# Kernel tuning notes

Measured on AMD Instinct MI355X. Metric: run time of the kernel, lower is better.

Reference implementation:

```python
import jax, jax.numpy as jnp
import numpy as np

N_DATA = 200000   # num_data
DIM = 128         # input_dim
BATCH = 40000     # minibatch receptive-field nodes (rows of output, cols of subsampled_support)
E_SUB = 320000    # nnz of subsampled_support (avg sampled degree 8)
E_SUP = 1280000   # nnz of support rows for the batch (avg degree 32)


def setup_inputs() -> dict:
    key = jax.random.key(0)
    ks = jax.random.split(key, 9)
    inputs = jax.random.normal(ks[0], (BATCH, DIM), dtype=jnp.float32)
    # old cached activations (non-trainable variable, but a float tensor)
    old_activation = jax.random.normal(ks[1], (N_DATA, DIM), dtype=jnp.float32)
    input_fields = jax.random.randint(ks[2], (BATCH,), 0, N_DATA, dtype=jnp.int32)
    # subsampled_support: sparse [BATCH, BATCH] in COO
    sub_rows = jax.random.randint(ks[3], (E_SUB,), 0, BATCH, dtype=jnp.int32)
    sub_cols = jax.random.randint(ks[4], (E_SUB,), 0, BATCH, dtype=jnp.int32)
    sub_vals = jax.random.uniform(ks[5], (E_SUB,), dtype=jnp.float32)
    # support: sparse [BATCH, N_DATA] in COO
    sup_rows = jax.random.randint(ks[6], (E_SUP,), 0, BATCH, dtype=jnp.int32)
    sup_cols = jax.random.randint(ks[7], (E_SUP,), 0, N_DATA, dtype=jnp.int32)
    sup_vals = jax.random.uniform(ks[8], (E_SUP,), dtype=jnp.float32)
    return {
        "inputs": inputs,
        "old_activation": old_activation,
        "input_fields": input_fields,
        "sub_rows": sub_rows,
        "sub_cols": sub_cols,
        "sub_vals": sub_vals,
        "sup_rows": sup_rows,
        "sup_cols": sup_cols,
        "sup_vals": sup_vals,
    }


def _spmm(rows, cols, vals, dense, num_rows):
    # sparse [num_rows, K] (COO) @ dense [K, D] -> [num_rows, D]
    return jax.ops.segment_sum(vals[:, None] * dense[cols], rows, num_segments=num_rows)


def reference(inputs, old_activation, input_fields, sub_rows, sub_cols, sub_vals,
              sup_rows, sup_cols, sup_vals):
    M = inputs.shape[0]
    old = old_activation[input_fields]                      # [B, D] gather
    norm = lambda x: jnp.sqrt(jnp.sum(jnp.square(x)))
    sim = jnp.sum(inputs * old) / norm(inputs) / norm(old)  # logged scalar (tf.Print)
    diff = inputs - old
    out = _spmm(sub_rows, sub_cols, sub_vals, diff, M) \
        + _spmm(sup_rows, sup_cols, sup_vals, old_activation, M)
    return out, sim
```

## Files before the change

kernel.cpp:

```cpp
#include <hip/hip_runtime.h>
#include <math.h>

#define DIM 128
#define TPB 256
#define PREP_GRID 2048
#define SUB_CAP 32
#define SUP_CAP 64
#define OVER_MAX 65536

__global__ void prep_bin_kernel(const float* __restrict__ inputs,
                                const float* __restrict__ old_act,
                                const int* __restrict__ fields,
                                const int* __restrict__ sub_rows, const int* __restrict__ sub_cols,
                                const float* __restrict__ sub_vals, int e_sub,
                                const int* __restrict__ sup_rows, const int* __restrict__ sup_cols,
                                const float* __restrict__ sup_vals, int e_sup,
                                int* __restrict__ cnt,
                                int2* __restrict__ pk_sub, int2* __restrict__ pk_sup,
                                int4* __restrict__ over,
                                float* __restrict__ partials, float* __restrict__ diff,
                                int use_diff, int nrows, int n2) {
    int tid = blockIdx.x * blockDim.x + threadIdx.x;
    int stride = gridDim.x * blockDim.x;
    int* over_cnt = cnt + 2 * nrows;

    float dot = 0.f, nx = 0.f, ny = 0.f;
    for (int i = tid; i < n2; i += stride) {
        int idx = i * 2;
        int b = idx >> 7, d = idx & (DIM - 1);
        float2 x = *(const float2*)(inputs + idx);
        int f = fields[b];
        float2 y = *(const float2*)(old_act + (size_t)f * DIM + d);
        dot += x.x * y.x + x.y * y.y;
        nx  += x.x * x.x + x.y * x.y;
        ny  += y.x * y.x + y.y * y.y;
        if (use_diff)
            *(float2*)(diff + idx) = make_float2(x.x - y.x, x.y - y.y);
    }
    int e_tot = e_sub + e_sup;
    for (int i = tid; i < e_tot; i += stride) {
        int r, c, sup; float v;
        if (i < e_sub) { r = sub_rows[i]; c = sub_cols[i]; v = sub_vals[i]; sup = 0; }
        else { int k = i - e_sub; r = sup_rows[k]; c = sup_cols[k]; v = sup_vals[k]; sup = 1; }
        int pos = atomicAdd(&cnt[sup ? nrows + r : r], 1);
        int cap = sup ? SUP_CAP : SUB_CAP;
        if (pos < cap) {
            int2* base = sup ? (pk_sup + (size_t)r * SUP_CAP) : (pk_sub + (size_t)r * SUB_CAP);
            base[pos] = make_int2(c, __float_as_int(v));
        } else {
            int op = atomicAdd(over_cnt, 1);
            if (op < OVER_MAX) over[op] = make_int4(r, c, __float_as_int(v), sup);
        }
    }
    for (int off = 32; off > 0; off >>= 1) {
        dot += __shfl_down(dot, off, 64);
        nx  += __shfl_down(nx,  off, 64);
        ny  += __shfl_down(ny,  off, 64);
    }
    __shared__ float s[3][4];
    int lane = threadIdx.x & 63, wv = threadIdx.x >> 6;
    if (lane == 0) { s[0][wv] = dot; s[1][wv] = nx; s[2][wv] = ny; }
    __syncthreads();
    if (threadIdx.x == 0) {
        float D = 0.f, NX = 0.f, NY = 0.f;
        for (int w = 0; w < 4; ++w) { D += s[0][w]; NX += s[1][w]; NY += s[2][w]; }
        partials[blockIdx.x * 3 + 0] = D;
        partials[blockIdx.x * 3 + 1] = NX;
        partials[blockIdx.x * 3 + 2] = NY;
    }
}

__global__ void row_bucket_kernel(const int* __restrict__ cnt,
                                  const int2* __restrict__ pk_sub, const int2* __restrict__ pk_sup,
                                  const float* __restrict__ diff,
                                  const float* __restrict__ inputs, const float* __restrict__ old_act,
                                  const int* __restrict__ fields,
                                  float* __restrict__ out, int nrows, int use_diff) {
    int wv = threadIdx.x >> 6, lane = threadIdx.x & 63;
    int r = blockIdx.x * (blockDim.x >> 6) + wv;
    if (r >= nrows) return;
    const int d0 = lane * 2;
    float a0 = 0.f, a1 = 0.f;

    {
        int e = cnt[r]; if (e > SUB_CAP) e = SUB_CAP;
        const int2* bp = pk_sub + (size_t)r * SUB_CAP;
        if (use_diff) {
            int j = 0;
            for (; j + 4 <= e; j += 4) {
                int2 p0 = bp[j], p1 = bp[j + 1], p2 = bp[j + 2], p3 = bp[j + 3];
                float2 y0 = *(const float2*)(diff + (size_t)p0.x * DIM + d0);
                float2 y1 = *(const float2*)(diff + (size_t)p1.x * DIM + d0);
                float2 y2 = *(const float2*)(diff + (size_t)p2.x * DIM + d0);
                float2 y3 = *(const float2*)(diff + (size_t)p3.x * DIM + d0);
                a0 += __int_as_float(p0.y) * y0.x; a1 += __int_as_float(p0.y) * y0.y;
                a0 += __int_as_float(p1.y) * y1.x; a1 += __int_as_float(p1.y) * y1.y;
                a0 += __int_as_float(p2.y) * y2.x; a1 += __int_as_float(p2.y) * y2.y;
                a0 += __int_as_float(p3.y) * y3.x; a1 += __int_as_float(p3.y) * y3.y;
            }
            for (; j < e; ++j) {
                int2 p = bp[j];
                float2 y = *(const float2*)(diff + (size_t)p.x * DIM + d0);
                a0 += __int_as_float(p.y) * y.x;
                a1 += __int_as_float(p.y) * y.y;
            }
        } else {
            for (int j = 0; j < e; ++j) {
                int2 p = bp[j];
                int c = p.x; float v = __int_as_float(p.y);
                int f = fields[c];
                float2 x = *(const float2*)(inputs  + (size_t)c * DIM + d0);
                float2 y = *(const float2*)(old_act + (size_t)f * DIM + d0);
                a0 += v * (x.x - y.x);
                a1 += v * (x.y - y.y);
            }
        }
    }
    {
        int e = cnt[nrows + r]; if (e > SUP_CAP) e = SUP_CAP;
        const int2* bp = pk_sup + (size_t)r * SUP_CAP;
        int j = 0;
        for (; j + 4 <= e; j += 4) {
            int2 p0 = bp[j], p1 = bp[j + 1], p2 = bp[j + 2], p3 = bp[j + 3];
            float2 y0 = *(const float2*)(old_act + (size_t)p0.x * DIM + d0);
            float2 y1 = *(const float2*)(old_act + (size_t)p1.x * DIM + d0);
            float2 y2 = *(const float2*)(old_act + (size_t)p2.x * DIM + d0);
            float2 y3 = *(const float2*)(old_act + (size_t)p3.x * DIM + d0);
            a0 += __int_as_float(p0.y) * y0.x; a1 += __int_as_float(p0.y) * y0.y;
            a0 += __int_as_float(p1.y) * y1.x; a1 += __int_as_float(p1.y) * y1.y;
            a0 += __int_as_float(p2.y) * y2.x; a1 += __int_as_float(p2.y) * y2.y;
            a0 += __int_as_float(p3.y) * y3.x; a1 += __int_as_float(p3.y) * y3.y;
        }
        for (; j < e; ++j) {
            int2 p = bp[j];
            float2 y = *(const float2*)(old_act + (size_t)p.x * DIM + d0);
            a0 += __int_as_float(p.y) * y.x;
            a1 += __int_as_float(p.y) * y.y;
        }
    }
    *(float2*)(out + (size_t)r * DIM + d0) = make_float2(a0, a1);
}

__global__ void tail_kernel(const float* __restrict__ partials, int np,
                            const int* __restrict__ cnt, const int4* __restrict__ over,
                            const float* __restrict__ diff,
                            const float* __restrict__ inputs, const float* __restrict__ old_act,
                            const int* __restrict__ fields,
                            float* __restrict__ out, int nrows, int n, int use_diff) {
    if (blockIdx.x == 0 && threadIdx.x < 64) {
        double dot = 0.0, nx = 0.0, ny = 0.0;
        for (int i = threadIdx.x; i < np; i += 64) {
            dot += (double)partials[i * 3 + 0];
            nx  += (double)partials[i * 3 + 1];
            ny  += (double)partials[i * 3 + 2];
        }
        for (int off = 32; off > 0; off >>= 1) {
            dot += __shfl_down(dot, off, 64);
            nx  += __shfl_down(nx,  off, 64);
            ny  += __shfl_down(ny,  off, 64);
        }
        if (threadIdx.x == 0)
            out[n] = (float)(dot / (sqrt(nx) * sqrt(ny)));
    }
    int no = cnt[2 * nrows]; if (no > OVER_MAX) no = OVER_MAX;
    int tid = blockIdx.x * blockDim.x + threadIdx.x;
    int stride = gridDim.x * blockDim.x;
    for (int i = tid; i < no; i += stride) {
        int4 t = over[i];
        int r = t.x, c = t.y, sup = t.w;
        float v = __int_as_float(t.z);
        for (int d = 0; d < DIM; ++d) {
            float term;
            if (sup) term = old_act[(size_t)c * DIM + d];
            else if (use_diff) term = diff[(size_t)c * DIM + d];
            else term = inputs[(size_t)c * DIM + d] - old_act[(size_t)fields[c] * DIM + d];
            atomicAdd(&out[(size_t)r * DIM + d], v * term);
        }
    }
}

__global__ void prep4_kernel(const float* __restrict__ inputs, const float* __restrict__ old_act,
                             const int* __restrict__ fields,
                             const int* __restrict__ sub_rows, int e_sub,
                             const int* __restrict__ sup_rows, int e_sup,
                             int* __restrict__ cnt, float* __restrict__ partials,
                             int nrows, int n2) {
    int tid = blockIdx.x * blockDim.x + threadIdx.x;
    int stride = gridDim.x * blockDim.x;
    float dot = 0.f, nx = 0.f, ny = 0.f;
    for (int i = tid; i < n2; i += stride) {
        int idx = i * 2;
        int b = idx >> 7, d = idx & (DIM - 1);
        float2 x = *(const float2*)(inputs + idx);
        int f = fields[b];
        float2 y = *(const float2*)(old_act + (size_t)f * DIM + d);
        dot += x.x * y.x + x.y * y.y;
        nx  += x.x * x.x + x.y * x.y;
        ny  += y.x * y.x + y.y * y.y;
    }
    int e_tot = e_sub + e_sup;
    for (int i = tid; i < e_tot; i += stride) {
        int r = (i < e_sub) ? sub_rows[i] : (nrows + sup_rows[i - e_sub]);
        atomicAdd(&cnt[r], 1);
    }
    for (int off = 32; off > 0; off >>= 1) {
        dot += __shfl_down(dot, off, 64);
        nx  += __shfl_down(nx,  off, 64);
        ny  += __shfl_down(ny,  off, 64);
    }
    __shared__ float s[3][4];
    int lane = threadIdx.x & 63, wv = threadIdx.x >> 6;
    if (lane == 0) { s[0][wv] = dot; s[1][wv] = nx; s[2][wv] = ny; }
    __syncthreads();
    if (threadIdx.x == 0) {
        float D = 0.f, NX = 0.f, NY = 0.f;
        for (int w = 0; w < 4; ++w) { D += s[0][w]; NX += s[1][w]; NY += s[2][w]; }
        partials[blockIdx.x * 3 + 0] = D;
        partials[blockIdx.x * 3 + 1] = NX;
        partials[blockIdx.x * 3 + 2] = NY;
    }
}

__global__ void finalize4_kernel(const float* __restrict__ partials, int np,
                                 float* __restrict__ out_sim) {
    double dot = 0.0, nx = 0.0, ny = 0.0;
    for (int i = threadIdx.x; i < np; i += 64) {
        dot += (double)partials[i * 3 + 0];
        nx  += (double)partials[i * 3 + 1];
        ny  += (double)partials[i * 3 + 2];
    }
    for (int off = 32; off > 0; off >>= 1) {
        dot += __shfl_down(dot, off, 64);
        nx  += __shfl_down(nx,  off, 64);
        ny  += __shfl_down(ny,  off, 64);
    }
    if (threadIdx.x == 0)
        *out_sim = (float)(dot / (sqrt(nx) * sqrt(ny)));
}

__global__ void scanA_kernel(const int* __restrict__ cnt, int* __restrict__ tmp,
                             int* __restrict__ bsum, int m) {
    __shared__ int s[256];
    int i = blockIdx.x * 256 + threadIdx.x;
    int v = (i < m) ? cnt[i] : 0;
    s[threadIdx.x] = v;
    __syncthreads();
    for (int d = 1; d < 256; d <<= 1) {
        int t = (threadIdx.x >= (unsigned)d) ? s[threadIdx.x - d] : 0;
        __syncthreads();
        s[threadIdx.x] += t;
        __syncthreads();
    }
    if (i < m) tmp[i] = s[threadIdx.x] - v;
    if (threadIdx.x == 255) bsum[blockIdx.x] = s[255];
}

__global__ void scanB_kernel(int* __restrict__ bsum, int* __restrict__ boff, int nb) {
    __shared__ int s[512];
    int v = (threadIdx.x < nb) ? bsum[threadIdx.x] : 0;
    s[threadIdx.x] = v;
    __syncthreads();
    for (int d = 1; d < 512; d <<= 1) {
        int t = (threadIdx.x >= (unsigned)d) ? s[threadIdx.x - d] : 0;
        __syncthreads();
        s[threadIdx.x] += t;
        __syncthreads();
    }
    if (threadIdx.x < nb) boff[threadIdx.x] = s[threadIdx.x] - v;
}

__global__ void scanC_kernel(const int* tmp, const int* __restrict__ boff,
                             int* __restrict__ off, int* cur, int m, int e_tot) {
    int i = blockIdx.x * 256 + threadIdx.x;
    if (i < m) {
        int o = tmp[i] + boff[i >> 8];
        off[i] = o;
        cur[i] = o;
    }
    if (i == 0) off[m] = e_tot;
}

__global__ void scatter4_kernel(const int* __restrict__ sub_rows, const int* __restrict__ sub_cols,
                                const float* __restrict__ sub_vals, int e_sub,
                                const int* __restrict__ sup_rows, const int* __restrict__ sup_cols,
                                const float* __restrict__ sup_vals, int e_sup,
                                int* __restrict__ cur, int2* __restrict__ pk, int nrows) {
    int i = blockIdx.x * blockDim.x + threadIdx.x;
    int e_tot = e_sub + e_sup;
    if (i >= e_tot) return;
    int r, c; float v;
    if (i < e_sub) { r = sub_rows[i]; c = sub_cols[i]; v = sub_vals[i]; }
    else { int k = i - e_sub; r = nrows + sup_rows[k]; c = sup_cols[k]; v = sup_vals[k]; }
    int pos = atomicAdd(&cur[r], 1);
    pk[pos] = make_int2(c, __float_as_int(v));
}

__global__ void row4_kernel(const int* __restrict__ off, const int2* __restrict__ pk,
                            const float* __restrict__ inputs, const float* __restrict__ old_act,
                            const int* __restrict__ fields, float* __restrict__ out, int nrows) {
    int wv = threadIdx.x >> 6, lane = threadIdx.x & 63;
    int r = blockIdx.x * (blockDim.x >> 6) + wv;
    if (r >= nrows) return;
    int d0 = lane * 2;
    float a0 = 0.f, a1 = 0.f;
    int b = off[r], e = off[r + 1];
    for (int j = b; j < e; ++j) {
        int2 p = pk[j];
        int c = p.x; float v = __int_as_float(p.y);
        int f = fields[c];
        float2 x = *(const float2*)(inputs  + (size_t)c * DIM + d0);
        float2 y = *(const float2*)(old_act + (size_t)f * DIM + d0);
        a0 += v * (x.x - y.x);
        a1 += v * (x.y - y.y);
    }
    b = off[nrows + r]; e = off[nrows + r + 1];
    for (int j = b; j < e; ++j) {
        int2 p = pk[j];
        int c = p.x; float v = __int_as_float(p.y);
        float2 y = *(const float2*)(old_act + (size_t)c * DIM + d0);
        a0 += v * y.x;
        a1 += v * y.y;
    }
    *(float2*)(out + (size_t)r * DIM + d0) = make_float2(a0, a1);
}

extern "C" void kernel_launch(void* const* d_in, const int* in_sizes, int n_in,
                              void* d_out, int out_size, void* d_ws, size_t ws_size,
                              hipStream_t stream) {
    const float* inputs   = (const float*)d_in[0];
    const float* old_act  = (const float*)d_in[1];
    const int*   fields   = (const int*)d_in[2];
    const int*   sub_rows = (const int*)d_in[3];
    const int*   sub_cols = (const int*)d_in[4];
    const float* sub_vals = (const float*)d_in[5];
    const int*   sup_rows = (const int*)d_in[6];
    const int*   sup_cols = (const int*)d_in[7];
    const float* sup_vals = (const float*)d_in[8];

    const int n     = in_sizes[0];
    const int nrows = n / DIM;
    const int e_sub = in_sizes[3];
    const int e_sup = in_sizes[6];
    const int e_tot = e_sub + e_sup;

    float* out = (float*)d_out;
    char*  ws  = (char*)d_ws;

    size_t off_part = 0;
    size_t off_cnt  = (PREP_GRID * 3 * 4 + 63) & ~(size_t)63;
    size_t off_over = (off_cnt + (size_t)(2 * nrows + 1) * 4 + 15) & ~(size_t)15;
    size_t off_psub = off_over + (size_t)OVER_MAX * 16;
    size_t off_psup = off_psub + (size_t)nrows * SUB_CAP * 8;
    size_t off_diff = off_psup + (size_t)nrows * SUP_CAP * 8;
    size_t need_base = off_diff;
    size_t need_diff = off_diff + (size_t)n * 4;

    if (ws_size >= need_base) {
        float* partials = (float*)(ws + off_part);
        int*   cnt      = (int*)(ws + off_cnt);
        int4*  over     = (int4*)(ws + off_over);
        int2*  pk_sub   = (int2*)(ws + off_psub);
        int2*  pk_sup   = (int2*)(ws + off_psup);
        float* diff     = (float*)(ws + off_diff);
        int use_diff    = (ws_size >= need_diff) ? 1 : 0;

        hipMemsetAsync(cnt, 0, (size_t)(2 * nrows + 1) * 4, stream);

        prep_bin_kernel<<<PREP_GRID, TPB, 0, stream>>>(
            inputs, old_act, fields,
            sub_rows, sub_cols, sub_vals, e_sub,
            sup_rows, sup_cols, sup_vals, e_sup,
            cnt, pk_sub, pk_sup, over, partials, diff, use_diff, nrows, n / 2);

        row_bucket_kernel<<<(nrows + 3) / 4, TPB, 0, stream>>>(
            cnt, pk_sub, pk_sup, diff, inputs, old_act, fields, out, nrows, use_diff);

        tail_kernel<<<32, TPB, 0, stream>>>(
            partials, PREP_GRID, cnt, over, diff, inputs, old_act, fields,
            out, nrows, n, use_diff);
        return;
    }

    const int m     = 2 * nrows;
    const int nblkA = (m + 255) / 256;
    size_t f_part = 0;
    size_t f_cnt  = (2048 * 3 * 4 + 63) & ~(size_t)63;
    size_t f_tmp  = f_cnt + (size_t)m * 4;
    size_t f_offs = f_tmp + (size_t)m * 4;
    size_t f_bsum = f_offs + (size_t)(m + 1) * 4;
    size_t f_boff = f_bsum + 4096;
    size_t f_pk   = (f_boff + 4096 + 7) & ~(size_t)7;
    size_t f_need = f_pk + (size_t)e_tot * 8;

    float* partials = (float*)(ws + f_part);
    int*   cnt      = (int*)(ws + f_cnt);
    int*   tmp      = (int*)(ws + f_tmp);
    int*   offs     = (int*)(ws + f_offs);
    int*   bsum     = (int*)(ws + f_bsum);
    int*   boff     = (int*)(ws + f_boff);
    int2*  pk       = (int2*)(ws + f_pk);

    if (ws_size >= f_need && nblkA <= 512) {
        hipMemsetAsync(cnt, 0, (size_t)m * 4, stream);
        prep4_kernel<<<2048, 256, 0, stream>>>(inputs, old_act, fields,
                                               sub_rows, e_sub, sup_rows, e_sup,
                                               cnt, partials, nrows, n / 2);
        scanA_kernel<<<nblkA, 256, 0, stream>>>(cnt, tmp, bsum, m);
        scanB_kernel<<<1, 512, 0, stream>>>(bsum, boff, nblkA);
        scanC_kernel<<<nblkA, 256, 0, stream>>>(tmp, boff, offs, tmp, m, e_tot);
        scatter4_kernel<<<(e_tot + 255) / 256, 256, 0, stream>>>(
            sub_rows, sub_cols, sub_vals, e_sub,
            sup_rows, sup_cols, sup_vals, e_sup, tmp, pk, nrows);
        row4_kernel<<<(nrows + 3) / 4, 256, 0, stream>>>(offs, pk, inputs, old_act,
                                                         fields, out, nrows);
        finalize4_kernel<<<1, 64, 0, stream>>>(partials, 2048, out + n);
    }
}
```

Measured before the change: 419.8 us.

## Partition COO binning by row across XCD groups and widen loads

The binning loop now splits blocks into 8 groups keyed on blockIdx low bits. Each group scans all edge rows but only inserts edges whose row matches its group, so atomics and bucket writes for a row stay on one XCD's L2. The cost is that every group rereads the row arrays, which is 8x traffic on the row indices. The prep gather now moves float4 instead of float2, and the row bucket kernel reads packed (col,val) pairs as int4 with the sup loop unrolled to 8 in-flight gathers.

```diff
diff --git a/kernel.cpp b/kernel.cpp
--- a/kernel.cpp
+++ b/kernel.cpp
@@ -7,6 +7,7 @@
 #define SUB_CAP 32
 #define SUP_CAP 64
 #define OVER_MAX 65536
+#define NXCD 8
 
 __global__ void prep_bin_kernel(const float* __restrict__ inputs,
                                 const float* __restrict__ old_act,
@@ -19,29 +20,38 @@
                                 int2* __restrict__ pk_sub, int2* __restrict__ pk_sup,
                                 int4* __restrict__ over,
                                 float* __restrict__ partials, float* __restrict__ diff,
-                                int use_diff, int nrows, int n2) {
+                                int use_diff, int nrows, int n4) {
     int tid = blockIdx.x * blockDim.x + threadIdx.x;
     int stride = gridDim.x * blockDim.x;
     int* over_cnt = cnt + 2 * nrows;
 
     float dot = 0.f, nx = 0.f, ny = 0.f;
-    for (int i = tid; i < n2; i += stride) {
-        int idx = i * 2;
+    for (int i = tid; i < n4; i += stride) {
+        int idx = i * 4;
         int b = idx >> 7, d = idx & (DIM - 1);
-        float2 x = *(const float2*)(inputs + idx);
+        float4 x = *(const float4*)(inputs + idx);
         int f = fields[b];
-        float2 y = *(const float2*)(old_act + (size_t)f * DIM + d);
-        dot += x.x * y.x + x.y * y.y;
-        nx  += x.x * x.x + x.y * x.y;
-        ny  += y.x * y.x + y.y * y.y;
+        float4 y = *(const float4*)(old_act + (size_t)f * DIM + d);
+        dot += x.x * y.x + x.y * y.y + x.z * y.z + x.w * y.w;
+        nx  += x.x * x.x + x.y * x.y + x.z * x.z + x.w * x.w;
+        ny  += y.x * y.x + y.y * y.y + y.z * y.z + y.w * y.w;
         if (use_diff)
-            *(float2*)(diff + idx) = make_float2(x.x - y.x, x.y - y.y);
-    }
+            *(float4*)(diff + idx) = make_float4(x.x - y.x, x.y - y.y, x.z - y.z, x.w - y.w);
+    }
+
     int e_tot = e_sub + e_sup;
-    for (int i = tid; i < e_tot; i += stride) {
-        int r, c, sup; float v;
-        if (i < e_sub) { r = sub_rows[i]; c = sub_cols[i]; v = sub_vals[i]; sup = 0; }
-        else { int k = i - e_sub; r = sup_rows[k]; c = sup_cols[k]; v = sup_vals[k]; sup = 1; }
+    int grp     = blockIdx.x & (NXCD - 1);
+    int gblk    = blockIdx.x >> 3;
+    int gtid    = gblk * blockDim.x + threadIdx.x;
+    int gstride = (gridDim.x >> 3) * blockDim.x;
+    for (int i = gtid; i < e_tot; i += gstride) {
+        int r, sup, k;
+        if (i < e_sub) { r = sub_rows[i]; sup = 0; k = i; }
+        else           { k = i - e_sub; r = sup_rows[k]; sup = 1; }
+        if ((r & (NXCD - 1)) != grp) continue;
+        int c; float v;
+        if (sup) { c = sup_cols[k]; v = sup_vals[k]; }
+        else     { c = sub_cols[k]; v = sub_vals[k]; }
         int pos = atomicAdd(&cnt[sup ? nrows + r : r], 1);
         int cap = sup ? SUP_CAP : SUB_CAP;
         if (pos < cap) {
@@ -52,6 +62,7 @@
             if (op < OVER_MAX) over[op] = make_int4(r, c, __float_as_int(v), sup);
         }
     }
+
     for (int off = 32; off > 0; off >>= 1) {
         dot += __shfl_down(dot, off, 64);
         nx  += __shfl_down(nx,  off, 64);
@@ -88,15 +99,16 @@
         if (use_diff) {
             int j = 0;
             for (; j + 4 <= e; j += 4) {
-                int2 p0 = bp[j], p1 = bp[j + 1], p2 = bp[j + 2], p3 = bp[j + 3];
-                float2 y0 = *(const float2*)(diff + (size_t)p0.x * DIM + d0);
-                float2 y1 = *(const float2*)(diff + (size_t)p1.x * DIM + d0);
-                float2 y2 = *(const float2*)(diff + (size_t)p2.x * DIM + d0);
-                float2 y3 = *(const float2*)(diff + (size_t)p3.x * DIM + d0);
-                a0 += __int_as_float(p0.y) * y0.x; a1 += __int_as_float(p0.y) * y0.y;
-                a0 += __int_as_float(p1.y) * y1.x; a1 += __int_as_float(p1.y) * y1.y;
-                a0 += __int_as_float(p2.y) * y2.x; a1 += __int_as_float(p2.y) * y2.y;
-                a0 += __int_as_float(p3.y) * y3.x; a1 += __int_as_float(p3.y) * y3.y;
+                int4 qa = *(const int4*)(bp + j);
+                int4 qb = *(const int4*)(bp + j + 2);
+                float2 y0 = *(const float2*)(diff + (size_t)qa.x * DIM + d0);
+                float2 y1 = *(const float2*)(diff + (size_t)qa.z * DIM + d0);
+                float2 y2 = *(const float2*)(diff + (size_t)qb.x * DIM + d0);
+                float2 y3 = *(const float2*)(diff + (size_t)qb.z * DIM + d0);
+                a0 += __int_as_float(qa.y) * y0.x; a1 += __int_as_float(qa.y) * y0.y;
+                a0 += __int_as_float(qa.w) * y1.x; a1 += __int_as_float(qa.w) * y1.y;
+                a0 += __int_as_float(qb.y) * y2.x; a1 += __int_as_float(qb.y) * y2.y;
+                a0 += __int_as_float(qb.w) * y3.x; a1 += __int_as_float(qb.w) * y3.y;
             }
             for (; j < e; ++j) {
                 int2 p = bp[j];
@@ -120,16 +132,27 @@
         int e = cnt[nrows + r]; if (e > SUP_CAP) e = SUP_CAP;
         const int2* bp = pk_sup + (size_t)r * SUP_CAP;
         int j = 0;
-        for (; j + 4 <= e; j += 4) {
-            int2 p0 = bp[j], p1 = bp[j + 1], p2 = bp[j + 2], p3 = bp[j + 3];
-            float2 y0 = *(const float2*)(old_act + (size_t)p0.x * DIM + d0);
-            float2 y1 = *(const float2*)(old_act + (size_t)p1.x * DIM + d0);
-            float2 y2 = *(const float2*)(old_act + (size_t)p2.x * DIM + d0);
-            float2 y3 = *(const float2*)(old_act + (size_t)p3.x * DIM + d0);
-            a0 += __int_as_float(p0.y) * y0.x; a1 += __int_as_float(p0.y) * y0.y;
-            a0 += __int_as_float(p1.y) * y1.x; a1 += __int_as_float(p1.y) * y1.y;
-            a0 += __int_as_float(p2.y) * y2.x; a1 += __int_as_float(p2.y) * y2.y;
-            a0 += __int_as_float(p3.y) * y3.x; a1 += __int_as_float(p3.y) * y3.y;
+        for (; j + 8 <= e; j += 8) {
+            int4 q0 = *(const int4*)(bp + j);
+            int4 q1 = *(const int4*)(bp + j + 2);
+            int4 q2 = *(const int4*)(bp + j + 4);
+            int4 q3 = *(const int4*)(bp + j + 6);
+            float2 y0 = *(const float2*)(old_act + (size_t)q0.x * DIM + d0);
+            float2 y1 = *(const float2*)(old_act + (size_t)q0.z * DIM + d0);
+            float2 y2 = *(const float2*)(old_act + (size_t)q1.x * DIM + d0);
+            float2 y3 = *(const float2*)(old_act + (size_t)q1.z * DIM + d0);
+            float2 y4 = *(const float2*)(old_act + (size_t)q2.x * DIM + d0);
+            float2 y5 = *(const float2*)(old_act + (size_t)q2.z * DIM + d0);
+            float2 y6 = *(const float2*)(old_act + (size_t)q3.x * DIM + d0);
+            float2 y7 = *(const float2*)(old_act + (size_t)q3.z * DIM + d0);
+            a0 += __int_as_float(q0.y) * y0.x; a1 += __int_as_float(q0.y) * y0.y;
+            a0 += __int_as_float(q0.w) * y1.x; a1 += __int_as_float(q0.w) * y1.y;
+            a0 += __int_as_float(q1.y) * y2.x; a1 += __int_as_float(q1.y) * y2.y;
+            a0 += __int_as_float(q1.w) * y3.x; a1 += __int_as_float(q1.w) * y3.y;
+            a0 += __int_as_float(q2.y) * y4.x; a1 += __int_as_float(q2.y) * y4.y;
+            a0 += __int_as_float(q2.w) * y5.x; a1 += __int_as_float(q2.w) * y5.y;
+            a0 += __int_as_float(q3.y) * y6.x; a1 += __int_as_float(q3.y) * y6.y;
+            a0 += __int_as_float(q3.w) * y7.x; a1 += __int_as_float(q3.w) * y7.y;
         }
         for (; j < e; ++j) {
             int2 p = bp[j];
@@ -370,7 +393,7 @@
             inputs, old_act, fields,
             sub_rows, sub_cols, sub_vals, e_sub,
             sup_rows, sup_cols, sup_vals, e_sup,
-            cnt, pk_sub, pk_sup, over, partials, diff, use_diff, nrows, n / 2);
+            cnt, pk_sub, pk_sup, over, partials, diff, use_diff, nrows, n / 4);
 
         row_bucket_kernel<<<(nrows + 3) / 4, TPB, 0, stream>>>(
             cnt, pk_sub, pk_sup, diff, inputs, old_act, fields, out, nrows, use_diff);
```

Measured after the change: 375.6 us. 1.12x faster.
